# Optimization experiments

Hardware: AMD Instinct MI355X
Metric: run time of the kernel (lower is better)

## Reference

```python
import jax, jax.numpy as jnp
import numpy as np

# Problem sizes (batched graph of G molecules)
N = 100_000   # total nodes
E = 400_000   # total directed edges
G = 2_500     # number of molecule graphs
K = 3         # len(idx_wo_smiles) -> zero rows inserted
NODE_F = 74   # graph_feats_shape[0]
EDGE_F = 12   # graph_feats_shape[1]
HID = 128     # hidden_feats = dim // 2
DIM = 256     # dim


def setup_inputs() -> dict:
    key = jax.random.key(0)
    ks = jax.random.split(key, 20)
    init = lambda k, shape, fan: (jax.random.normal(k, shape, jnp.float32) / np.sqrt(fan)).astype(jnp.float32)

    node_feats = jax.random.normal(ks[0], (N, NODE_F), jnp.float32)
    edge_feats = jax.random.normal(ks[1], (E, EDGE_F), jnp.float32)  # passed but unused by GCN
    src = jax.random.randint(ks[2], (E,), 0, N)
    dst = jax.random.randint(ks[3], (E,), 0, N)
    # sorted graph ids, every graph non-empty (~40 atoms each)
    graph_ids = (jnp.arange(N) * G) // N
    idx_wo_smiles = jnp.arange(K)

    return {
        'node_feats': node_feats,
        'edge_feats': edge_feats,
        'W1': init(ks[4], (NODE_F, HID), NODE_F), 'b1': jnp.zeros((HID,), jnp.float32),
        'Wr1': init(ks[5], (NODE_F, HID), NODE_F), 'br1': jnp.zeros((HID,), jnp.float32),
        'W2': init(ks[6], (HID, HID), HID), 'b2': jnp.zeros((HID,), jnp.float32),
        'Wr2': init(ks[7], (HID, HID), HID), 'br2': jnp.zeros((HID,), jnp.float32),
        'w_atom': init(ks[8], (HID, 1), HID), 'b_atom': jnp.zeros((1,), jnp.float32),
        'Wp1': init(ks[9], (2 * HID, HID), 2 * HID), 'bp1': jnp.zeros((HID,), jnp.float32),
        'Wp2': init(ks[10], (HID, DIM), HID), 'bp2': jnp.zeros((DIM,), jnp.float32),
        'src': src, 'dst': dst, 'graph_ids': graph_ids, 'idx_wo_smiles': idx_wo_smiles,
    }


def reference(node_feats, edge_feats, W1, b1, Wr1, br1, W2, b2, Wr2, br2,
              w_atom, b_atom, Wp1, bp1, Wp2, bp2, src, dst, graph_ids, idx_wo_smiles):
    n = node_feats.shape[0]
    ones_e = jnp.ones(src.shape[0], jnp.float32)
    out_deg = jax.ops.segment_sum(ones_e, src, num_segments=n)
    in_deg = jax.ops.segment_sum(ones_e, dst, num_segments=n)
    norm_s = jax.lax.rsqrt(jnp.maximum(out_deg, 1.0))  # [N]
    norm_d = jax.lax.rsqrt(jnp.maximum(in_deg, 1.0))   # [N]

    def gcn_layer(h, W, b, Wr, br):
        # GraphConv(norm='both'): D^-1/2 A D^-1/2 h W + b, with relu activation
        m = h[src] * norm_s[src][:, None]                       # [E, F] gather
        agg = jax.ops.segment_sum(m, dst, num_segments=n)       # [N, F] scatter-add
        gc = jax.nn.relu((agg * norm_d[:, None]) @ W + b)
        res = jax.nn.relu(h @ Wr + br)                          # residual connection
        return gc + res

    h = gcn_layer(node_feats, W1, b1, Wr1, br1)   # [N, HID]
    h = gcn_layer(h, W2, b2, Wr2, br2)            # [N, HID]

    # WeightedSumAndMax readout per molecule
    aw = jax.nn.sigmoid(h @ w_atom + b_atom)                          # [N, 1]
    hsum = jax.ops.segment_sum(h * aw, graph_ids, num_segments=G)     # [G, HID]
    hmax = jax.ops.segment_max(h, graph_ids, num_segments=G)          # [G, HID]
    gfeat = jnp.concatenate([hsum, hmax], axis=1)                     # [G, 2*HID]

    latent = jax.nn.relu(gfeat @ Wp1 + bp1) @ Wp2 + bp2               # [G, DIM]

    # Insert zero rows at idx_wo_smiles (sorted ascending -> final positions)
    total = G + idx_wo_smiles.shape[0]
    zero_mask = jnp.zeros((total,), bool).at[idx_wo_smiles].set(True)
    keep = jnp.nonzero(~zero_mask, size=G)[0]
    out = jnp.zeros((total, latent.shape[1]), latent.dtype).at[keep].set(latent)
    return out
```

## Files before the change

kernel.cpp:

```cpp
#include <hip/hip_runtime.h>
#include <hip/hip_bf16.h>
#include <stdint.h>

#define NODE_F 74
#define HID 128
#define DIM 256

typedef __hip_bfloat16 bf16;
typedef unsigned int u32;
typedef unsigned short u16;

typedef short s16x8 __attribute__((ext_vector_type(8)));
typedef __bf16 bf16x8 __attribute__((ext_vector_type(8)));
typedef float f32x4 __attribute__((ext_vector_type(4)));

__device__ __forceinline__ float rdl(float v, int l){
  return __int_as_float(__builtin_amdgcn_readlane(__float_as_int(v), l));
}
__device__ __forceinline__ float2 bfpair(u32 u){
  float2 r;
  r.x = __uint_as_float(u << 16);
  r.y = __uint_as_float(u & 0xffff0000u);
  return r;
}
__device__ __forceinline__ u32 packbf(float a, float b){
  u32 lo = (u32)__bfloat16_as_ushort(__float2bfloat16(a));
  u32 hi = (u32)__bfloat16_as_ushort(__float2bfloat16(b));
  return lo | (hi << 16);
}
__device__ __forceinline__ u16 bfbits(float a){
  return __bfloat16_as_ushort(__float2bfloat16(a));
}

__global__ void k_deg_prep(const int* __restrict__ src, const int* __restrict__ dst_,
                           float* __restrict__ outdeg_f, int* __restrict__ indeg, int E_,
                           const float* __restrict__ W1, const float* __restrict__ Wr1,
                           const float* __restrict__ W2, const float* __restrict__ Wr2,
                           u16* __restrict__ Bp1, u16* __restrict__ Bp2){
  int e = blockIdx.x*256 + threadIdx.x;
  if (e < E_){
    atomicAdd(&outdeg_f[src[e]], 1.0f);
    atomicAdd(&indeg[dst_[e]], 1);
  }
  int idx = e;
  if (idx < 57344){
    const float* W; u16* dstp; int S, Ktrue, loc;
    if      (idx < 12288){ W = W1;  dstp = Bp1;          S = 3; Ktrue = NODE_F; loc = idx; }
    else if (idx < 24576){ W = Wr1; dstp = Bp1 + 12288;  S = 3; Ktrue = NODE_F; loc = idx - 12288; }
    else if (idx < 40960){ W = W2;  dstp = Bp2;          S = 4; Ktrue = HID;    loc = idx - 24576; }
    else                 { W = Wr2; dstp = Bp2 + 16384;  S = 4; Ktrue = HID;    loc = idx - 40960; }
    const int el  = loc & 7;
    const int l   = (loc >> 3) & 63;
    const int rem = loc >> 9;
    const int s   = rem % S;
    const int t   = rem / S;
    const int k   = s*32 + (l >> 4)*8 + el;
    const int c   = t*16 + (l & 15);
    const float v = (k < Ktrue) ? W[(size_t)k*HID + c] : 0.f;
    dstp[loc] = bfbits(v);
  }
}

__global__ __launch_bounds__(256) void k_scan_a(const int* __restrict__ indeg,
                                                float* __restrict__ norm_s,
                                                float* __restrict__ norm_d,
                                                int* __restrict__ bsum, int n){
  __shared__ int red[256];
  const int base = blockIdx.x*1024 + threadIdx.x*4;
  int s = 0;
  #pragma unroll
  for (int i = 0; i < 4; ++i){
    const int idx = base + i;
    if (idx < n){
      const int d = indeg[idx];
      s += d;
      norm_d[idx] = rsqrtf(fmaxf((float)d, 1.0f));
      norm_s[idx] = rsqrtf(fmaxf(norm_s[idx], 1.0f));
    }
  }
  red[threadIdx.x] = s;
  __syncthreads();
  #pragma unroll
  for (int off = 128; off; off >>= 1){
    if (threadIdx.x < off) red[threadIdx.x] += red[threadIdx.x + off];
    __syncthreads();
  }
  if (threadIdx.x == 0) bsum[blockIdx.x] = red[0];
}

__global__ __launch_bounds__(1024) void k_scan_b(int* __restrict__ bsum, int nb){
  __shared__ int part[1024];
  __shared__ int carry;
  if (threadIdx.x == 0) carry = 0;
  __syncthreads();
  for (int c0 = 0; c0 < nb; c0 += 1024){
    const int tid = threadIdx.x, idx = c0 + tid;
    part[tid] = (idx < nb) ? bsum[idx] : 0;
    __syncthreads();
    for (int off = 1; off < 1024; off <<= 1){
      const int t = (tid >= off) ? part[tid-off] : 0;
      __syncthreads();
      part[tid] += t;
      __syncthreads();
    }
    if (idx < nb) bsum[idx] = carry + ((tid == 0) ? 0 : part[tid-1]);
    __syncthreads();
    if (tid == 0) carry += part[1023];
    __syncthreads();
  }
}

__global__ __launch_bounds__(256) void k_scan_c(int* __restrict__ indeg,
                                                const int* __restrict__ bsum,
                                                int* __restrict__ row_ptr, int n){
  __shared__ int part[256];
  const int base = blockIdx.x*1024 + threadIdx.x*4;
  int v[4]; int s = 0;
  #pragma unroll
  for (int i = 0; i < 4; ++i){
    const int idx = base + i;
    v[i] = (idx < n) ? indeg[idx] : 0;
    s += v[i];
  }
  part[threadIdx.x] = s;
  __syncthreads();
  for (int off = 1; off < 256; off <<= 1){
    const int t = (threadIdx.x >= off) ? part[threadIdx.x-off] : 0;
    __syncthreads();
    part[threadIdx.x] += t;
    __syncthreads();
  }
  int run = bsum[blockIdx.x] + ((threadIdx.x == 0) ? 0 : part[threadIdx.x-1]);
  #pragma unroll
  for (int i = 0; i < 4; ++i){
    const int idx = base + i;
    if (idx < n){
      row_ptr[idx] = run;
      run += v[i];
      indeg[idx] = 0;
    }
    if (idx == n-1) row_ptr[n] = run;
  }
}

__global__ void k_fill(const int* __restrict__ src, const int* __restrict__ dst,
                       const int* __restrict__ row_ptr, int* __restrict__ cursor,
                       int* __restrict__ col, int E_){
  int e = blockIdx.x*256 + threadIdx.x;
  if (e < E_){
    int d = dst[e];
    int pos = row_ptr[d] + atomicAdd(&cursor[d], 1);
    col[pos] = src[e];
  }
}

__global__ __launch_bounds__(256) void k_gather1(
    const float* __restrict__ x0, const int* __restrict__ row_ptr,
    const int* __restrict__ col, const float* __restrict__ norm_s,
    const float* __restrict__ norm_d, u32* __restrict__ ag1, int n){
  const int lane = threadIdx.x & 63;
  const int row  = blockIdx.x*4 + (threadIdx.x >> 6);
  if (row >= n) return;
  const int p0 = row_ptr[row], p1 = row_ptr[row+1];
  const bool act = (lane < 37);
  const float* xb = x0 + 2*lane;
  float a0 = 0.f, a1 = 0.f;
  int p = p0;
  #pragma unroll 1
  for (; p + 3 < p1; p += 4){
    const int s0 = col[p], s1 = col[p+1], s2 = col[p+2], s3 = col[p+3];
    const float n0 = norm_s[s0], n1 = norm_s[s1], n2 = norm_s[s2], n3 = norm_s[s3];
    float2 v0{0.f,0.f}, v1{0.f,0.f}, v2{0.f,0.f}, v3{0.f,0.f};
    if (act){
      v0 = *(const float2*)&xb[(size_t)s0*NODE_F];
      v1 = *(const float2*)&xb[(size_t)s1*NODE_F];
      v2 = *(const float2*)&xb[(size_t)s2*NODE_F];
      v3 = *(const float2*)&xb[(size_t)s3*NODE_F];
    }
    a0 = fmaf(v0.x,n0, fmaf(v1.x,n1, fmaf(v2.x,n2, fmaf(v3.x,n3, a0))));
    a1 = fmaf(v0.y,n0, fmaf(v1.y,n1, fmaf(v2.y,n2, fmaf(v3.y,n3, a1))));
  }
  const int rem = p1 - p;
  if (rem > 0){
    const int s0 = col[p];
    int s1 = s0, s2 = s0;
    float n1 = 0.f, n2 = 0.f;
    const float n0 = norm_s[s0];
    if (rem > 1){ s1 = col[p+1]; n1 = norm_s[s1]; }
    if (rem > 2){ s2 = col[p+2]; n2 = norm_s[s2]; }
    float2 v0{0.f,0.f}, v1{0.f,0.f}, v2{0.f,0.f};
    if (act){
      v0 = *(const float2*)&xb[(size_t)s0*NODE_F];
      v1 = *(const float2*)&xb[(size_t)s1*NODE_F];
      v2 = *(const float2*)&xb[(size_t)s2*NODE_F];
    }
    a0 = fmaf(v0.x,n0, fmaf(v1.x,n1, fmaf(v2.x,n2, a0)));
    a1 = fmaf(v0.y,n0, fmaf(v1.y,n1, fmaf(v2.y,n2, a1)));
  }
  if (lane < 48){
    const float nd = norm_d[row];
    ag1[(size_t)row*48 + lane] = packbf(a0*nd, a1*nd);
  }
}

__global__ __launch_bounds__(256) void k_gather2(
    const u32* __restrict__ h1u, const int* __restrict__ row_ptr,
    const int* __restrict__ col, const float* __restrict__ norm_s,
    const float* __restrict__ norm_d, u32* __restrict__ ag2, int n){
  const int lane = threadIdx.x & 63;
  const int row  = blockIdx.x*4 + (threadIdx.x >> 6);
  if (row >= n) return;
  const int p0 = row_ptr[row], p1 = row_ptr[row+1];
  const u32* hb = h1u + lane;
  float a0 = 0.f, a1 = 0.f;
  int p = p0;
  #pragma unroll 1
  for (; p + 3 < p1; p += 4){
    const int s0 = col[p], s1 = col[p+1], s2 = col[p+2], s3 = col[p+3];
    const float n0 = norm_s[s0], n1 = norm_s[s1], n2 = norm_s[s2], n3 = norm_s[s3];
    const u32 u0 = hb[(size_t)s0*64];
    const u32 u1 = hb[(size_t)s1*64];
    const u32 u2 = hb[(size_t)s2*64];
    const u32 u3 = hb[(size_t)s3*64];
    const float2 f0 = bfpair(u0), f1 = bfpair(u1), f2 = bfpair(u2), f3 = bfpair(u3);
    a0 = fmaf(f0.x,n0, fmaf(f1.x,n1, fmaf(f2.x,n2, fmaf(f3.x,n3, a0))));
    a1 = fmaf(f0.y,n0, fmaf(f1.y,n1, fmaf(f2.y,n2, fmaf(f3.y,n3, a1))));
  }
  const int rem = p1 - p;
  if (rem > 0){
    const int s0 = col[p];
    int s1 = s0, s2 = s0;
    float n1 = 0.f, n2 = 0.f;
    const float n0 = norm_s[s0];
    if (rem > 1){ s1 = col[p+1]; n1 = norm_s[s1]; }
    if (rem > 2){ s2 = col[p+2]; n2 = norm_s[s2]; }
    const u32 u0 = hb[(size_t)s0*64];
    const u32 u1 = hb[(size_t)s1*64];
    const u32 u2 = hb[(size_t)s2*64];
    const float2 f0 = bfpair(u0), f1 = bfpair(u1), f2 = bfpair(u2);
    a0 = fmaf(f0.x,n0, fmaf(f1.x,n1, fmaf(f2.x,n2, a0)));
    a1 = fmaf(f0.y,n0, fmaf(f1.y,n1, fmaf(f2.y,n2, a1)));
  }
  const float nd = norm_d[row];
  ag2[(size_t)row*64 + lane] = packbf(a0*nd, a1*nd);
}

__global__ __launch_bounds__(256) void k_ggemm1(
    const u16* __restrict__ ag1, const float* __restrict__ x0,
    const u16* __restrict__ Bp, const float* __restrict__ bg_,
    const float* __restrict__ br_, u16* __restrict__ h1, int n){
  const int lane = threadIdx.x & 63;
  const int wid  = threadIdx.x >> 6;
  const int jg = lane & 15, kg = lane >> 4;
  const int r0 = blockIdx.x*64 + wid*16;
  const int row = r0 + jg;
  const bool rok = row < n;
  const int kb = kg*8;
  const int rA = rok ? row : (n-1);

  bf16x8 ag[3], ar[3];
  #pragma unroll
  for (int s = 0; s < 3; ++s)
    ag[s] = __builtin_bit_cast(bf16x8, *(const s16x8*)&ag1[(size_t)rA*96 + s*32 + kb]);
  {
    const float* px = x0 + (size_t)rA*NODE_F;
    #pragma unroll
    for (int s = 0; s < 2; ++s)
      #pragma unroll
      for (int e = 0; e < 8; e += 2){
        const float2 w = *(const float2*)&px[s*32 + kb + e];
        ar[s][e]   = (__bf16)w.x;
        ar[s][e+1] = (__bf16)w.y;
      }
    #pragma unroll
    for (int e = 0; e < 8; ++e) ar[2][e] = (__bf16)0.f;
    if (kg == 0){
      #pragma unroll
      for (int e = 0; e < 8; e += 2){
        const float2 w = *(const float2*)&px[64 + e];
        ar[2][e]   = (__bf16)w.x;
        ar[2][e+1] = (__bf16)w.y;
      }
    } else if (kg == 1){
      const float2 w = *(const float2*)&px[72];
      ar[2][0] = (__bf16)w.x;
      ar[2][1] = (__bf16)w.y;
    }
  }

  f32x4 accg[8], accr[8];
  #pragma unroll
  for (int t = 0; t < 8; ++t){
    accg[t] = f32x4{0.f,0.f,0.f,0.f};
    accr[t] = f32x4{0.f,0.f,0.f,0.f};
  }
  constexpr int FR1 = 8*3*512;
  #pragma unroll
  for (int s = 0; s < 3; ++s){
    #pragma unroll
    for (int t = 0; t < 8; ++t){
      const bf16x8 bg = __builtin_bit_cast(bf16x8,
          *(const s16x8*)&Bp[((t*3 + s)*64 + lane)*8]);
      const bf16x8 br = __builtin_bit_cast(bf16x8,
          *(const s16x8*)&Bp[FR1 + ((t*3 + s)*64 + lane)*8]);
      accg[t] = __builtin_amdgcn_mfma_f32_16x16x32_bf16(ag[s], bg, accg[t], 0,0,0);
      accr[t] = __builtin_amdgcn_mfma_f32_16x16x32_bf16(ar[s], br, accr[t], 0,0,0);
    }
  }

  const int rowb = r0 + 4*kg;
  #pragma unroll
  for (int t = 0; t < 8; ++t){
    const int colc = t*16 + jg;
    const float bgv = bg_[colc], brv = br_[colc];
    #pragma unroll
    for (int r = 0; r < 4; ++r){
      const int row2 = rowb + r;
      if (row2 < n){
        const float o = fmaxf(accg[t][r] + bgv, 0.f) + fmaxf(accr[t][r] + brv, 0.f);
        h1[(size_t)row2*HID + colc] = bfbits(o);
      }
    }
  }
}

__global__ __launch_bounds__(256) void k_ggemm2(
    const u16* __restrict__ ag2, const u16* __restrict__ h1,
    const u16* __restrict__ Bp, const float* __restrict__ bg_,
    const float* __restrict__ br_,
    const float* __restrict__ w_atom, const float* __restrict__ b_atom,
    const int* __restrict__ gid,
    float* __restrict__ hsum, u32* __restrict__ hmax, int n){
  const int lane = threadIdx.x & 63;
  const int wid  = threadIdx.x >> 6;
  const int jg = lane & 15, kg = lane >> 4;
  const int r0 = blockIdx.x*64 + wid*16;
  const int row = r0 + jg;
  const bool rok = row < n;
  const int kb = kg*8;
  const int rA = rok ? row : (n-1);

  f32x4 accg[8], accr[8];
  #pragma unroll
  for (int t = 0; t < 8; ++t){
    accg[t] = f32x4{0.f,0.f,0.f,0.f};
    accr[t] = f32x4{0.f,0.f,0.f,0.f};
  }
  constexpr int FR2 = 8*4*512;
  #pragma unroll
  for (int s = 0; s < 4; ++s){
    const bf16x8 agf = __builtin_bit_cast(bf16x8,
        *(const s16x8*)&ag2[(size_t)rA*HID + s*32 + kb]);
    const bf16x8 arf = __builtin_bit_cast(bf16x8,
        *(const s16x8*)&h1[(size_t)rA*HID + s*32 + kb]);
    #pragma unroll
    for (int t = 0; t < 8; ++t){
      const bf16x8 bg = __builtin_bit_cast(bf16x8,
          *(const s16x8*)&Bp[((t*4 + s)*64 + lane)*8]);
      const bf16x8 br = __builtin_bit_cast(bf16x8,
          *(const s16x8*)&Bp[FR2 + ((t*4 + s)*64 + lane)*8]);
      accg[t] = __builtin_amdgcn_mfma_f32_16x16x32_bf16(agf, bg, accg[t], 0,0,0);
      accr[t] = __builtin_amdgcn_mfma_f32_16x16x32_bf16(arf, br, accr[t], 0,0,0);
    }
  }

  float o[8][4];
  #pragma unroll
  for (int t = 0; t < 8; ++t){
    const int colc = t*16 + jg;
    const float bgv = bg_[colc], brv = br_[colc];
    #pragma unroll
    for (int r = 0; r < 4; ++r)
      o[t][r] = fmaxf(accg[t][r] + bgv, 0.f) + fmaxf(accr[t][r] + brv, 0.f);
  }
  if (r0 < n){
    float wa[8];
    #pragma unroll
    for (int t = 0; t < 8; ++t) wa[t] = w_atom[t*16 + jg];
    const float ba = b_atom[0];
    const int rowb = r0 + 4*kg;
    float awv[4]; int gidr[4];
    #pragma unroll
    for (int r = 0; r < 4; ++r){
      const int row2 = rowb + r;
      float dot = 0.f;
      #pragma unroll
      for (int t = 0; t < 8; ++t) dot = fmaf(o[t][r], wa[t], dot);
      dot += __shfl_xor(dot, 1);
      dot += __shfl_xor(dot, 2);
      dot += __shfl_xor(dot, 4);
      dot += __shfl_xor(dot, 8);
      awv[r]  = 1.0f/(1.0f + __expf(-(dot + ba)));
      gidr[r] = (row2 < n) ? gid[row2] : -1;
    }
    const int rhi    = (r0 + 15 < n) ? (r0 + 15) : (n - 1);
    const int gfirst = gid[r0];
    const int glast  = gid[rhi];
    for (int g = gfirst; g <= glast; ++g){
      #pragma unroll
      for (int t = 0; t < 8; ++t){
        float sv = 0.f, mv = 0.f;
        #pragma unroll
        for (int r = 0; r < 4; ++r){
          const bool in = (gidr[r] == g);
          sv += in ? o[t][r]*awv[r] : 0.f;
          mv  = in ? fmaxf(mv, o[t][r]) : mv;
        }
        sv += __shfl_xor(sv, 16);
        sv += __shfl_xor(sv, 32);
        mv  = fmaxf(mv, __shfl_xor(mv, 16));
        mv  = fmaxf(mv, __shfl_xor(mv, 32));
        if (lane < 16){
          atomicAdd(&hsum[(size_t)g*HID + t*16 + jg], sv);
          atomicMax(&hmax[(size_t)g*HID + t*16 + jg], __float_as_uint(mv));
        }
      }
    }
  }
}

__global__ __launch_bounds__(256) void k_mlp(
    const float* __restrict__ hsum, const float* __restrict__ hmaxf,
    const float* __restrict__ Wp1, const float* __restrict__ bp1,
    const float* __restrict__ Wp2, const float* __restrict__ bp2,
    const int* __restrict__ idxw, int K_,
    float* __restrict__ out, int G_){
  const int lane = threadIdx.x & 63;
  const int row = blockIdx.x*4 + (threadIdx.x >> 6);
  if (blockIdx.x == 0){
    for (int j = 0; j < K_; ++j){
      const int zr = idxw[j];
      for (int i = threadIdx.x; i < DIM; i += 256)
        out[(size_t)zr*DIM + i] = 0.f;
    }
  }
  if (row >= G_) return;
  const int c = lane*2;
  float ra0 = hsum [(size_t)row*HID + lane];
  float ra1 = hsum [(size_t)row*HID + 64 + lane];
  float ra2 = hmaxf[(size_t)row*HID + lane];
  float ra3 = hmaxf[(size_t)row*HID + 64 + lane];
  float a0 = 0.f, a1 = 0.f;
  #pragma unroll 4
  for (int k = 0; k < 64; ++k){
    const float v0 = rdl(ra0,k), v1 = rdl(ra1,k), v2 = rdl(ra2,k), v3 = rdl(ra3,k);
    const float2 w0 = *(const float2*)&Wp1[(size_t)(k      )*HID + c];
    const float2 w1 = *(const float2*)&Wp1[(size_t)(k +  64)*HID + c];
    const float2 w2 = *(const float2*)&Wp1[(size_t)(k + 128)*HID + c];
    const float2 w3 = *(const float2*)&Wp1[(size_t)(k + 192)*HID + c];
    a0 = fmaf(v0,w0.x, fmaf(v1,w1.x, fmaf(v2,w2.x, fmaf(v3,w3.x, a0))));
    a1 = fmaf(v0,w0.y, fmaf(v1,w1.y, fmaf(v2,w2.y, fmaf(v3,w3.y, a1))));
  }
  const float h0  = fmaxf(a0 + bp1[c],   0.f);
  const float h1v = fmaxf(a1 + bp1[c+1], 0.f);
  const int c4 = lane*4;
  float acc0=0.f, acc1=0.f, acc2=0.f, acc3=0.f;
  #pragma unroll 4
  for (int j = 0; j < 64; ++j){
    const float he = rdl(h0, j);
    const float ho = rdl(h1v, j);
    const float4 we = *(const float4*)&Wp2[(size_t)(2*j  )*DIM + c4];
    const float4 wo = *(const float4*)&Wp2[(size_t)(2*j+1)*DIM + c4];
    acc0 = fmaf(he,we.x, fmaf(ho,wo.x, acc0));
    acc1 = fmaf(he,we.y, fmaf(ho,wo.y, acc1));
    acc2 = fmaf(he,we.z, fmaf(ho,wo.z, acc2));
    acc3 = fmaf(he,we.w, fmaf(ho,wo.w, acc3));
  }
  int orow = row;
  for (int j = 0; j < K_; ++j){ if (idxw[j] <= orow) orow++; }
  float* po = out + (size_t)orow*DIM + c4;
  po[0] = acc0 + bp2[c4];
  po[1] = acc1 + bp2[c4+1];
  po[2] = acc2 + bp2[c4+2];
  po[3] = acc3 + bp2[c4+3];
}

extern "C" void kernel_launch(void* const* d_in, const int* in_sizes, int n_in,
                              void* d_out, int out_size, void* d_ws, size_t ws_size,
                              hipStream_t stream){
  (void)n_in; (void)ws_size;
  const float* x0     = (const float*)d_in[0];
  const float* W1     = (const float*)d_in[2];
  const float* b1     = (const float*)d_in[3];
  const float* Wr1    = (const float*)d_in[4];
  const float* br1    = (const float*)d_in[5];
  const float* W2     = (const float*)d_in[6];
  const float* b2     = (const float*)d_in[7];
  const float* Wr2    = (const float*)d_in[8];
  const float* br2    = (const float*)d_in[9];
  const float* w_atom = (const float*)d_in[10];
  const float* b_atom = (const float*)d_in[11];
  const float* Wp1    = (const float*)d_in[12];
  const float* bp1    = (const float*)d_in[13];
  const float* Wp2    = (const float*)d_in[14];
  const float* bp2    = (const float*)d_in[15];
  const int* src  = (const int*)d_in[16];
  const int* dst  = (const int*)d_in[17];
  const int* gid  = (const int*)d_in[18];
  const int* idxw = (const int*)d_in[19];

  const int N_ = in_sizes[0] / NODE_F;
  const int E_ = in_sizes[16];
  const int K_ = in_sizes[19];
  const int G_ = out_size / DIM - K_;

  u16*   h1     = (u16*)d_ws;
  float* norm_d = (float*)(h1 + (size_t)N_*HID);
  float* norm_s = norm_d + N_;
  float* hsum   = norm_s + N_;
  float* hmaxv  = hsum + (size_t)G_*HID;
  int*   indeg  = (int*)(hmaxv + (size_t)G_*HID);
  int*   row_ptr= indeg + N_;
  int*   col    = row_ptr + ((N_ + 4) & ~3);
  int*   bsum   = col + ((E_ + 4) & ~3);
  const int nscan = (N_ + 1023)/1024;
  uintptr_t aggp = ((uintptr_t)(bsum + nscan) + 255) & ~(uintptr_t)255;
  u32* aggu = (u32*)aggp;

  u16*   Bp1    = (u16*)d_out;
  u16*   Bp2    = Bp1 + 2*12288;

  hipMemsetAsync(norm_s, 0, ((size_t)2*N_ + (size_t)2*G_*HID)*sizeof(float), stream);

  k_deg_prep<<<(E_+255)/256, 256, 0, stream>>>(src, dst, norm_s, indeg, E_,
                                               W1, Wr1, W2, Wr2, Bp1, Bp2);
  k_scan_a  <<<nscan, 256, 0, stream>>>(indeg, norm_s, norm_d, bsum, N_);
  k_scan_b  <<<1, 1024, 0, stream>>>(bsum, nscan);
  k_scan_c  <<<nscan, 256, 0, stream>>>(indeg, bsum, row_ptr, N_);
  k_fill    <<<(E_+255)/256, 256, 0, stream>>>(src, dst, row_ptr, indeg, col, E_);

  const int nb  = (N_ + 63) / 64;
  const int nbw = (N_ + 3) / 4;
  k_gather1<<<nbw, 256, 0, stream>>>(x0, row_ptr, col, norm_s, norm_d, aggu, N_);
  k_ggemm1 <<<nb, 256, 0, stream>>>((const u16*)aggu, x0, Bp1, b1, br1, h1, N_);
  k_gather2<<<nbw, 256, 0, stream>>>((const u32*)h1, row_ptr, col, norm_s, norm_d,
                                     aggu, N_);
  k_ggemm2 <<<nb, 256, 0, stream>>>((const u16*)aggu, h1, Bp2, b2, br2,
                                    w_atom, b_atom, gid, hsum, (u32*)hmaxv, N_);

  k_mlp<<<(G_+3)/4, 256, 0, stream>>>(hsum, hmaxv, Wp1, bp1, Wp2, bp2,
                                      idxw, K_, (float*)d_out, G_);
}
```

Baseline: 373.9 us.

## Pre-scale node features to bf16 and gather two rows per wavefront

The fill kernel now also converts node features to a padded bf16 copy pre-multiplied by norm_s, so layer-1 gather reads 4-byte packed pairs per lane and skips the per-neighbour norm_s loads. Both gather kernels now process two destination rows per wavefront, with interleaved 4-wide neighbour batches, to expose more memory-level parallelism. A fallback to the old fp32 path is kept when the workspace is too small. The extra conversion pass adds traffic and bf16 rounding of the inputs before aggregation.

```diff
diff --git a/kernel.cpp b/kernel.cpp
--- a/kernel.cpp
+++ b/kernel.cpp
@@ -143,18 +143,155 @@
   }
 }
 
-__global__ void k_fill(const int* __restrict__ src, const int* __restrict__ dst,
-                       const int* __restrict__ row_ptr, int* __restrict__ cursor,
-                       int* __restrict__ col, int E_){
+__global__ void k_fill_conv(const int* __restrict__ src, const int* __restrict__ dst,
+                            const int* __restrict__ row_ptr, int* __restrict__ cursor,
+                            int* __restrict__ col, int E_,
+                            const float* __restrict__ x0,
+                            const float* __restrict__ norm_s,
+                            u32* __restrict__ x0bf, int n, int do_conv){
   int e = blockIdx.x*256 + threadIdx.x;
   if (e < E_){
     int d = dst[e];
     int pos = row_ptr[d] + atomicAdd(&cursor[d], 1);
     col[pos] = src[e];
   }
-}
-
-__global__ __launch_bounds__(256) void k_gather1(
+  if (do_conv){
+    const int tot = n*48;
+    if (e < tot){
+      const int r = e/48, l = e - r*48;
+      const int f0 = 2*l, f1 = 2*l + 1;
+      const float ns = norm_s[r];
+      const float u0 = (f0 < NODE_F) ? ns*x0[(size_t)r*NODE_F + f0] : 0.f;
+      const float u1 = (f1 < NODE_F) ? ns*x0[(size_t)r*NODE_F + f1] : 0.f;
+      x0bf[e] = packbf(u0, u1);
+    }
+  }
+}
+
+__global__ __launch_bounds__(256, 8) void k_gather1b(
+    const u32* __restrict__ x0bf, const int* __restrict__ row_ptr,
+    const int* __restrict__ col, const float* __restrict__ norm_d,
+    u32* __restrict__ ag1, int n){
+  const int lane = threadIdx.x & 63;
+  const int wv   = (blockIdx.x*256 + threadIdx.x) >> 6;
+  const int r0   = wv*2;
+  if (r0 >= n) return;
+  int p[2], e[2];
+  p[0] = row_ptr[r0]; e[0] = row_ptr[r0+1];
+  const bool ok1 = (r0+1) < n;
+  p[1] = ok1 ? e[0] : 0;
+  e[1] = ok1 ? row_ptr[r0+2] : 0;
+  const bool act = (lane < 48);
+  const u32* xb = x0bf + lane;
+  float a0[2] = {0.f,0.f}, a1[2] = {0.f,0.f};
+  while ((p[0] < e[0]) | (p[1] < e[1])){
+    int c[2], s[2][4];
+    #pragma unroll
+    for (int i = 0; i < 2; ++i){
+      int d = e[i] - p[i];
+      c[i] = (d > 4) ? 4 : ((d < 0) ? 0 : d);
+      if (c[i] > 0){
+        #pragma unroll
+        for (int j = 0; j < 4; ++j)
+          s[i][j] = col[p[i] + ((j < c[i]) ? j : (c[i]-1))];
+      }
+    }
+    u32 v[2][4];
+    #pragma unroll
+    for (int i = 0; i < 2; ++i){
+      #pragma unroll
+      for (int j = 0; j < 4; ++j) v[i][j] = 0u;
+      if (c[i] > 0 && act){
+        #pragma unroll
+        for (int j = 0; j < 4; ++j){
+          const u32 t = xb[(size_t)s[i][j]*48];
+          v[i][j] = (j < c[i]) ? t : 0u;
+        }
+      }
+    }
+    #pragma unroll
+    for (int i = 0; i < 2; ++i){
+      const float2 f0 = bfpair(v[i][0]), f1 = bfpair(v[i][1]);
+      const float2 f2 = bfpair(v[i][2]), f3 = bfpair(v[i][3]);
+      a0[i] += (f0.x + f1.x) + (f2.x + f3.x);
+      a1[i] += (f0.y + f1.y) + (f2.y + f3.y);
+      p[i] += c[i];
+    }
+  }
+  if (lane < 48){
+    #pragma unroll
+    for (int i = 0; i < 2; ++i){
+      const int row = r0 + i;
+      if (row < n){
+        const float nd = norm_d[row];
+        ag1[(size_t)row*48 + lane] = packbf(a0[i]*nd, a1[i]*nd);
+      }
+    }
+  }
+}
+
+__global__ __launch_bounds__(256, 8) void k_gather2b(
+    const u32* __restrict__ h1u, const int* __restrict__ row_ptr,
+    const int* __restrict__ col, const float* __restrict__ norm_s,
+    const float* __restrict__ norm_d, u32* __restrict__ ag2, int n){
+  const int lane = threadIdx.x & 63;
+  const int wv   = (blockIdx.x*256 + threadIdx.x) >> 6;
+  const int r0   = wv*2;
+  if (r0 >= n) return;
+  int p[2], e[2];
+  p[0] = row_ptr[r0]; e[0] = row_ptr[r0+1];
+  const bool ok1 = (r0+1) < n;
+  p[1] = ok1 ? e[0] : 0;
+  e[1] = ok1 ? row_ptr[r0+2] : 0;
+  const u32* hb = h1u + lane;
+  float a0[2] = {0.f,0.f}, a1[2] = {0.f,0.f};
+  while ((p[0] < e[0]) | (p[1] < e[1])){
+    int c[2], s[2][4];
+    #pragma unroll
+    for (int i = 0; i < 2; ++i){
+      int d = e[i] - p[i];
+      c[i] = (d > 4) ? 4 : ((d < 0) ? 0 : d);
+      if (c[i] > 0){
+        #pragma unroll
+        for (int j = 0; j < 4; ++j)
+          s[i][j] = col[p[i] + ((j < c[i]) ? j : (c[i]-1))];
+      }
+    }
+    float nw[2][4];
+    u32 v[2][4];
+    #pragma unroll
+    for (int i = 0; i < 2; ++i){
+      #pragma unroll
+      for (int j = 0; j < 4; ++j){ nw[i][j] = 0.f; v[i][j] = 0u; }
+      if (c[i] > 0){
+        #pragma unroll
+        for (int j = 0; j < 4; ++j) nw[i][j] = (j < c[i]) ? norm_s[s[i][j]] : 0.f;
+        #pragma unroll
+        for (int j = 0; j < 4; ++j) v[i][j] = hb[(size_t)s[i][j]*64];
+      }
+    }
+    #pragma unroll
+    for (int i = 0; i < 2; ++i){
+      const float2 f0 = bfpair(v[i][0]), f1 = bfpair(v[i][1]);
+      const float2 f2 = bfpair(v[i][2]), f3 = bfpair(v[i][3]);
+      a0[i] = fmaf(f0.x, nw[i][0], fmaf(f1.x, nw[i][1],
+              fmaf(f2.x, nw[i][2], fmaf(f3.x, nw[i][3], a0[i]))));
+      a1[i] = fmaf(f0.y, nw[i][0], fmaf(f1.y, nw[i][1],
+              fmaf(f2.y, nw[i][2], fmaf(f3.y, nw[i][3], a1[i]))));
+      p[i] += c[i];
+    }
+  }
+  #pragma unroll
+  for (int i = 0; i < 2; ++i){
+    const int row = r0 + i;
+    if (row < n){
+      const float nd = norm_d[row];
+      ag2[(size_t)row*64 + lane] = packbf(a0[i]*nd, a1[i]*nd);
+    }
+  }
+}
+
+__global__ __launch_bounds__(256) void k_gather1f(
     const float* __restrict__ x0, const int* __restrict__ row_ptr,
     const int* __restrict__ col, const float* __restrict__ norm_s,
     const float* __restrict__ norm_d, u32* __restrict__ ag1, int n){
@@ -203,7 +340,7 @@
   }
 }
 
-__global__ __launch_bounds__(256) void k_gather2(
+__global__ __launch_bounds__(256) void k_gather2f(
     const u32* __restrict__ h1u, const int* __restrict__ row_ptr,
     const int* __restrict__ col, const float* __restrict__ norm_s,
     const float* __restrict__ norm_d, u32* __restrict__ ag2, int n){
@@ -478,7 +615,7 @@
 extern "C" void kernel_launch(void* const* d_in, const int* in_sizes, int n_in,
                               void* d_out, int out_size, void* d_ws, size_t ws_size,
                               hipStream_t stream){
-  (void)n_in; (void)ws_size;
+  (void)n_in;
   const float* x0     = (const float*)d_in[0];
   const float* W1     = (const float*)d_in[2];
   const float* b1     = (const float*)d_in[3];
@@ -516,6 +653,10 @@
   const int nscan = (N_ + 1023)/1024;
   uintptr_t aggp = ((uintptr_t)(bsum + nscan) + 255) & ~(uintptr_t)255;
   u32* aggu = (u32*)aggp;
+  uintptr_t x0bfp = aggp + (size_t)N_*64*sizeof(u32);
+  u32* x0bf = (u32*)x0bfp;
+  const size_t need_bf = (x0bfp + (size_t)N_*48*sizeof(u32)) - (uintptr_t)d_ws;
+  const bool use_bf = (ws_size >= need_bf);
 
   u16*   Bp1    = (u16*)d_out;
   u16*   Bp2    = Bp1 + 2*12288;
@@ -527,16 +668,30 @@
   k_scan_a  <<<nscan, 256, 0, stream>>>(indeg, norm_s, norm_d, bsum, N_);
   k_scan_b  <<<1, 1024, 0, stream>>>(bsum, nscan);
   k_scan_c  <<<nscan, 256, 0, stream>>>(indeg, bsum, row_ptr, N_);
-  k_fill    <<<(E_+255)/256, 256, 0, stream>>>(src, dst, row_ptr, indeg, col, E_);
-
-  const int nb  = (N_ + 63) / 64;
-  const int nbw = (N_ + 3) / 4;
-  k_gather1<<<nbw, 256, 0, stream>>>(x0, row_ptr, col, norm_s, norm_d, aggu, N_);
-  k_ggemm1 <<<nb, 256, 0, stream>>>((const u16*)aggu, x0, Bp1, b1, br1, h1, N_);
-  k_gather2<<<nbw, 256, 0, stream>>>((const u32*)h1, row_ptr, col, norm_s, norm_d,
-                                     aggu, N_);
-  k_ggemm2 <<<nb, 256, 0, stream>>>((const u16*)aggu, h1, Bp2, b2, br2,
-                                    w_atom, b_atom, gid, hsum, (u32*)hmaxv, N_);
+
+  const int conv_tot = use_bf ? (N_*48 > E_ ? N_*48 : E_) : E_;
+  k_fill_conv<<<(conv_tot+255)/256, 256, 0, stream>>>(
+      src, dst, row_ptr, indeg, col, E_, x0, norm_s,
+      use_bf ? x0bf : aggu, N_, use_bf ? 1 : 0);
+
+  const int nb   = (N_ + 63) / 64;
+  const int nbw  = (N_ + 3) / 4;
+  const int nbw2 = (N_ + 7) / 8;
+  if (use_bf){
+    k_gather1b<<<nbw2, 256, 0, stream>>>(x0bf, row_ptr, col, norm_d, aggu, N_);
+  } else {
+    k_gather1f<<<nbw, 256, 0, stream>>>(x0, row_ptr, col, norm_s, norm_d, aggu, N_);
+  }
+  k_ggemm1<<<nb, 256, 0, stream>>>((const u16*)aggu, x0, Bp1, b1, br1, h1, N_);
+  if (use_bf){
+    k_gather2b<<<nbw2, 256, 0, stream>>>((const u32*)h1, row_ptr, col, norm_s,
+                                         norm_d, aggu, N_);
+  } else {
+    k_gather2f<<<nbw, 256, 0, stream>>>((const u32*)h1, row_ptr, col, norm_s,
+                                        norm_d, aggu, N_);
+  }
+  k_ggemm2<<<nb, 256, 0, stream>>>((const u16*)aggu, h1, Bp2, b2, br2,
+                                   w_atom, b_atom, gid, hsum, (u32*)hmaxv, N_);
 
   k_mlp<<<(G_+3)/4, 256, 0, stream>>>(hsum, hmaxv, Wp1, bp1, Wp2, bp2,
                                       idxw, K_, (float*)d_out, G_);
```

Result: no change. 367.5 us (-1.7%).
